# Kernel optimization log

Hardware: AMD Instinct MI355X
Metric: run time of the kernel (lower is better)

Reference implementation:

```python
import jax, jax.numpy as jnp
import numpy as np

NUM_NODES = 324
IN_DIM, HID_DIM, OUT_DIM = 128, 256, 64
BN_EPS = 1e-5
HUB_COLS = [7, 9, 24, 45, 59, 62, 63, 66, 67, 69, 70, 73, 74, 76, 77, 80, 81, 84,
            95, 97, 99, 114, 116, 118, 143, 147, 150, 152, 156, 158, 159, 163, 167, 171]


def _adj_norm() -> jnp.ndarray:
    """D^{-1/2} A D^{-1/2} for the fixed 324-node template graph (edge weights = 1)."""
    adj = np.eye(NUM_NODES, dtype=np.float32)
    cols = np.array(HUB_COLS)
    for r in range(300, NUM_NODES):
        adj[r, cols] = 1.0
        adj[cols, r] = 1.0
    deg = adj.sum(axis=1)
    dinv = 1.0 / np.sqrt(deg)
    return jnp.asarray(adj * dinv[:, None] * dinv[None, :])


def setup_inputs() -> dict:
    key = jax.random.key(0)
    ks = jax.random.split(key, 6)
    batch = 1024
    x = jax.random.normal(ks[0], (batch, NUM_NODES, IN_DIM), dtype=jnp.float32)
    # Xavier-uniform linear weights (PyG GCNConv lin has weight [out, in]), zero bias
    lim1 = float(np.sqrt(6.0 / (IN_DIM + HID_DIM)))
    W1 = jax.random.uniform(ks[1], (HID_DIM, IN_DIM), jnp.float32, -lim1, lim1)
    b1 = jnp.zeros((HID_DIM,), jnp.float32)
    lim2 = float(np.sqrt(6.0 / (HID_DIM + OUT_DIM)))
    W2 = jax.random.uniform(ks[2], (OUT_DIM, HID_DIM), jnp.float32, -lim2, lim2)
    b2 = jnp.zeros((OUT_DIM,), jnp.float32)
    # BatchNorm1d(hidden_dim) params + running stats (inference mode)
    gamma = jax.random.uniform(ks[3], (HID_DIM,), jnp.float32, 0.5, 1.5)
    beta = 0.1 * jax.random.normal(ks[4], (HID_DIM,), jnp.float32)
    running_mean = jnp.zeros((HID_DIM,), jnp.float32)
    running_var = jnp.ones((HID_DIM,), jnp.float32)
    return {"x": x, "W1": W1, "b1": b1, "W2": W2, "b2": b2,
            "gamma": gamma, "beta": beta,
            "running_mean": running_mean, "running_var": running_var,
            "adj_norm": _adj_norm()}


def reference(x, W1, b1, W2, b2, gamma, beta, running_mean, running_var, adj_norm):
    # Layer 0: GCNConv = aggregate(norm_adj, x @ W^T) + b  (batched over b)
    h = jnp.einsum("bnf,hf->bnh", x, W1)               # lin
    h = jnp.einsum("nm,bmh->bnh", adj_norm, h) + b1    # normalized scatter-aggregate
    h = jnp.where(h >= 0, h, 0.01 * h)                 # leaky_relu(0.01)
    # dropout: identity at inference
    h = (h - running_mean) * gamma * jax.lax.rsqrt(running_var + BN_EPS) + beta
    # Layer 1 (final): GCNConv only
    out = jnp.einsum("bnh,oh->bno", h, W2)
    out = jnp.einsum("nm,bmo->bno", adj_norm, out) + b2
    return out
```

## Files before the change

### kernel.cpp

```cpp
#include <hip/hip_runtime.h>

#define NN   324
#define INF  128
#define HID  256
#define OUTF 64

#define DINV_R 0.16903085f
#define DINV_H 0.2f

#define W1B_OFF 655360
#define W2B_OFF 671744
#define C2_OFF  679936

typedef float  f32x16 __attribute__((ext_vector_type(16)));
typedef short  short8 __attribute__((ext_vector_type(8)));

__constant__ int HUBC[34] = {7, 9, 24, 45, 59, 62, 63, 66, 67, 69, 70, 73, 74, 76,
                             77, 80, 81, 84, 95, 97, 99, 114, 116, 118, 143, 147,
                             150, 152, 156, 158, 159, 163, 167, 171};

#define HW0 ((1ULL<<7)|(1ULL<<9)|(1ULL<<24)|(1ULL<<45)|(1ULL<<59)|(1ULL<<62)|(1ULL<<63))
#define HW1 ((1ULL<<2)|(1ULL<<3)|(1ULL<<5)|(1ULL<<6)|(1ULL<<9)|(1ULL<<10)|(1ULL<<12)|(1ULL<<13)| \
             (1ULL<<16)|(1ULL<<17)|(1ULL<<20)|(1ULL<<31)|(1ULL<<33)|(1ULL<<35)|(1ULL<<50)|(1ULL<<52)|(1ULL<<54))
#define HW2 ((1ULL<<15)|(1ULL<<19)|(1ULL<<22)|(1ULL<<24)|(1ULL<<28)|(1ULL<<30)|(1ULL<<31)| \
             (1ULL<<35)|(1ULL<<39)|(1ULL<<43))

__device__ __forceinline__ bool is_hub(int n) {
    if (n >= 192) return false;
    unsigned long long w = (n < 64) ? HW0 : (n < 128 ? HW1 : HW2);
    return (w >> (n & 63)) & 1ULL;
}
__device__ __forceinline__ unsigned int f2bf1(float f) {
    unsigned int u = __builtin_bit_cast(unsigned int, f);
    return (u + 0x7fffu + ((u >> 16) & 1u)) >> 16;
}
__device__ __forceinline__ float bf2f(unsigned short h) {
    return __builtin_bit_cast(float, (unsigned int)h << 16);
}
__device__ __forceinline__ unsigned int f2bf2(float lo, float hi) {
    return f2bf1(lo) | (f2bf1(hi) << 16);
}
__device__ __forceinline__ uint4 pack8(float4 a, float4 b) {
    uint4 r;
    r.x = f2bf2(a.x, a.y); r.y = f2bf2(a.z, a.w);
    r.z = f2bf2(b.x, b.y); r.w = f2bf2(b.z, b.w);
    return r;
}
__device__ __forceinline__ short8 as_s8(uint4 u) {
    union { uint4 u; short8 s; } t; t.u = u; return t.s;
}

__global__ __launch_bounds__(256) void gcn_k00(
    const float* __restrict__ W1, const float* __restrict__ W2,
    const float* __restrict__ gamma, const float* __restrict__ beta,
    const float* __restrict__ rmean, const float* __restrict__ rvar,
    float* __restrict__ ws)
{
    const int blk = blockIdx.x, tid = threadIdx.x;
    if (blk < 16) {
        int p = blk * 256 + tid;
        int l31 = p & 31, hi = (p >> 5) & 1, ks = (p >> 6) & 7, htc = p >> 9;
        int h = htc * 32 + l31;
        int k0 = ks * 16 + hi * 8;
        const float4* s = (const float4*)(W1 + (size_t)h * INF + k0);
        ((uint4*)(ws + W1B_OFF))[p] = pack8(s[0], s[1]);
    } else if (blk < 24) {
        int p = (blk - 16) * 256 + tid;
        int l31 = p & 31, hi = (p >> 5) & 1, ot = (p >> 6) & 1, hs = (p >> 7) & 1, htc = p >> 8;
        int o = ot * 32 + l31;
        int h0 = htc * 32 + hs * 16 + hi * 8;
        float4 a = *(const float4*)(W2 + (size_t)o * HID + h0);
        float4 b = *(const float4*)(W2 + (size_t)o * HID + h0 + 4);
        float4 ga = *(const float4*)(gamma + h0), gb = *(const float4*)(gamma + h0 + 4);
        float4 va = *(const float4*)(rvar + h0),  vb = *(const float4*)(rvar + h0 + 4);
        a.x *= ga.x * rsqrtf(va.x + 1e-5f);  a.y *= ga.y * rsqrtf(va.y + 1e-5f);
        a.z *= ga.z * rsqrtf(va.z + 1e-5f);  a.w *= ga.w * rsqrtf(va.w + 1e-5f);
        b.x *= gb.x * rsqrtf(vb.x + 1e-5f);  b.y *= gb.y * rsqrtf(vb.y + 1e-5f);
        b.z *= gb.z * rsqrtf(vb.z + 1e-5f);  b.w *= gb.w * rsqrtf(vb.w + 1e-5f);
        ((uint4*)(ws + W2B_OFF))[p] = pack8(a, b);
    } else {
        if (tid < 64) {
            float s = 0.f;
            for (int h = 0; h < HID; ++h) {
                float sc  = gamma[h] * rsqrtf(rvar[h] + 1e-5f);
                float off = beta[h] - rmean[h] * sc;
                s += off * W2[(size_t)tid * HID + h];
            }
            ws[C2_OFF + tid] = s;
        }
    }
}

__global__ __launch_bounds__(256, 3) void gcn_k0(
    const float* __restrict__ x,  const float* __restrict__ b1,
    const float* __restrict__ W2, const float* __restrict__ gamma,
    const float* __restrict__ beta, const float* __restrict__ rmean,
    const float* __restrict__ rvar, float* __restrict__ ws)
{
    __shared__ uint4 Xs[16 * 67];
    __shared__ float sv1[2][256];
    __shared__ float vpart[2][2][256];
    __shared__ float vHl[2][256];

    const int tid = threadIdx.x, lane = tid & 63, w = tid >> 6;
    const int mt = w >> 1, nh = w & 1, l31 = lane & 31, hi = lane >> 5;
    const int b = blockIdx.x;
    const float* xb = x + (size_t)b * NN * INF;
    float* wsb = ws + (size_t)b * 640;
    const uint4* W1B2q = (const uint4*)(ws + W1B_OFF);

    for (int p = tid; p < 64 * 16; p += 256) {
        int lr = p >> 4, kg = p & 15;
        uint4 v = {0u, 0u, 0u, 0u};
        if (lr < 58) {
            int gr = (lr < 24) ? 300 + lr : HUBC[lr - 24];
            const float4* s = (const float4*)(xb + (size_t)gr * INF + kg * 8);
            v = pack8(s[0], s[1]);
        }
        Xs[kg * 67 + lr] = v;
    }
    __syncthreads();

    if (tid < 128) {
        int kg = tid >> 3, sub = tid & 7;
        const unsigned short* xs = (const unsigned short*)Xs;
        float s1 = 0.f, s2 = 0.f;
        for (int lr = 0; lr < 24; ++lr)  s1 += bf2f(xs[(kg * 67 + lr) * 8 + sub]);
        for (int lr = 24; lr < 58; ++lr) s2 += bf2f(xs[(kg * 67 + lr) * 8 + sub]);
        unsigned short* xw = (unsigned short*)Xs;
        xw[(kg * 67 + 58) * 8 + sub] = (unsigned short)f2bf1(s1 * DINV_R);
        xw[(kg * 67 + 59) * 8 + sub] = (unsigned short)f2bf1(s2 * DINV_H);
    }
    __syncthreads();

    f32x16 acc[4];
#pragma unroll
    for (int i = 0; i < 4; ++i)
#pragma unroll
        for (int j = 0; j < 16; ++j) acc[i][j] = 0.f;

#pragma unroll
    for (int ks = 0; ks < 8; ++ks) {
        short8 af = as_s8(Xs[(2 * ks + hi) * 67 + mt * 32 + l31]);
#pragma unroll
        for (int ntl = 0; ntl < 4; ++ntl) {
            short8 bf = as_s8(W1B2q[((nh * 4 + ntl) * 8 + ks) * 64 + lane]);
            acc[ntl] = __builtin_amdgcn_mfma_f32_32x32x16_bf16(af, bf, acc[ntl], 0, 0, 0);
        }
    }

    if (mt == 1 && hi == 0) {
#pragma unroll
        for (int ntl = 0; ntl < 4; ++ntl) {
            int col = nh * 128 + ntl * 32 + l31;
            float r58 = acc[ntl][14], r59 = acc[ntl][15];
            sv1[0][col] = r58;  sv1[1][col] = r59;
            wsb[col] = r58;     wsb[256 + col] = r59;
        }
    }
    __syncthreads();

    float p1[4] = {0.f, 0.f, 0.f, 0.f}, p2[4] = {0.f, 0.f, 0.f, 0.f};
#pragma unroll
    for (int ntl = 0; ntl < 4; ++ntl) {
        int col = nh * 128 + ntl * 32 + l31;
        float bias  = b1[col];
        float scale = gamma[col] * rsqrtf(rvar[col] + 1e-5f);
        float off   = beta[col] - rmean[col] * scale;
        float svA = sv1[0][col], svB = sv1[1][col];
#pragma unroll
        for (int q = 0; q < 16; ++q) {
            int lr = mt * 32 + (q & 3) + 8 * (q >> 2) + 4 * hi;
            bool isR = lr < 24, isH = (lr >= 24 && lr < 58);
            float d   = isR ? DINV_R : (isH ? DINV_H : 0.f);
            float oth = isR ? svB : svA;
            float v = d * d * acc[ntl][q] + d * oth + bias;
            v = fmaxf(v, 0.01f * v);
            float z = v * scale + off;
            p1[ntl] += isR ? DINV_R * z : 0.f;
            p2[ntl] += isH ? DINV_H * z : 0.f;
        }
    }
#pragma unroll
    for (int ntl = 0; ntl < 4; ++ntl) {
        p1[ntl] += __shfl_xor(p1[ntl], 32);
        p2[ntl] += __shfl_xor(p2[ntl], 32);
    }
    if (hi == 0) {
#pragma unroll
        for (int ntl = 0; ntl < 4; ++ntl) {
            int col = nh * 128 + ntl * 32 + l31;
            vpart[mt][0][col] = p1[ntl];
            vpart[mt][1][col] = p2[ntl];
        }
    }
    __syncthreads();
    for (int i = tid; i < 512; i += 256) {
        int which = i >> 8, col = i & 255;
        vHl[which][col] = vpart[0][which][col] + vpart[1][which][col];
    }
    __syncthreads();

    if (tid < 128) {
        int vr = tid >> 6, oc = tid & 63;
        const float* w2r = W2 + (size_t)oc * HID;
        float s = 0.f;
        for (int k = 0; k < 256; k += 8) {
#pragma unroll
            for (int i = 0; i < 8; ++i) s += vHl[vr][k + i] * w2r[k + i];
        }
        wsb[512 + vr * 64 + oc] = s;
    }
}

#define PSTR 33
#define LDS_XW  0
#define LDS_B1  33792
#define LDS_ST  34816
#define LDS_E2  36864
#define LDS_K1  37888
__global__ __launch_bounds__(256, 4) void gcn_k1(
    const float* __restrict__ x,  const float* __restrict__ b1,
    const float* __restrict__ b2, const float* __restrict__ ws,
    float* __restrict__ out)
{
    extern __shared__ char smem[];
    const int tid = threadIdx.x, lane = tid & 63, w = tid >> 6;
    const int l31 = lane & 31, hi = lane >> 5;
    uint4*  Xw  = (uint4*)(smem + LDS_XW) + w * (16 * PSTR);
    float*  eb1 = (float*)(smem + LDS_B1);
    float2* est = (float2*)(smem + LDS_ST);
    float4* e2t = (float4*)(smem + LDS_E2);

    const int bid = blockIdx.x;
    const int b = bid / 3, m3 = bid - b * 3;
    const int row0 = m3 * 128 + w * 32;
    const float* xb  = x + ((size_t)b * NN + row0) * INF;
    const float* wsb = ws + (size_t)b * 640;
    const uint4* W1q = (const uint4*)(ws + W1B_OFF);
    const uint4* W2q = (const uint4*)(ws + W2B_OFF);

    eb1[tid] = b1[tid];
    est[tid] = make_float2(wsb[tid], wsb[256 + tid]);
    if (tid < 64)
        e2t[tid] = make_float4(ws[C2_OFF + tid], wsb[512 + tid], wsb[576 + tid], b2[tid]);

    float tx, ty, tz;
    {
        int gr = row0 + l31;
        if (gr >= NN)        { tx = 0.f;               ty = 0.f;    tz = 0.f;    }
        else if (gr >= 300)  { tx = DINV_R * DINV_R;   ty = 0.f;    tz = DINV_R; }
        else if (is_hub(gr)) { tx = DINV_H * DINV_H;   ty = DINV_H; tz = 0.f;    }
        else                 { tx = 1.f;               ty = 0.f;    tz = 0.f;    }
    }
    const bool anyspec = __ballot((ty != 0.f) || (tz != 0.f)) != 0ULL;

#pragma unroll
    for (int i = 0; i < 8; ++i) {
        int p = lane + i * 64;
        int n = p >> 4, kg = p & 15;
        uint4 v = {0u, 0u, 0u, 0u};
        if (row0 + n < NN) {
            const float4* s = (const float4*)(xb + (size_t)n * INF + kg * 8);
            v = pack8(s[0], s[1]);
        }
        Xw[kg * PSTR + n] = v;
    }
    __syncthreads();

    f32x16 acc2a, acc2b;
#pragma unroll
    for (int j = 0; j < 16; ++j) { acc2a[j] = 0.f; acc2b[j] = 0.f; }

#pragma unroll
    for (int hc = 0; hc < 4; ++hc) {
#pragma unroll
        for (int j = 0; j < 2; ++j) {
            const int htc = hc * 2 + j;
            f32x16 acc1;
#pragma unroll
            for (int q = 0; q < 16; ++q) acc1[q] = 0.f;
            const uint4* w1 = W1q + (size_t)(htc * 8) * 64 + lane;
#pragma unroll
            for (int ks = 0; ks < 8; ++ks) {
                short8 bX = as_s8(Xw[(2 * ks + hi) * PSTR + l31]);
                acc1 = __builtin_amdgcn_mfma_f32_32x32x16_bf16(
                           as_s8(w1[ks * 64]), bX, acc1, 0, 0, 0);
            }
            float z[16];
            if (anyspec) {
#pragma unroll
                for (int q = 0; q < 16; ++q) {
                    int h = htc * 32 + (q & 3) + 8 * (q >> 2) + 4 * hi;
                    float2 st = est[h];
                    float v = tx * acc1[q] + ty * st.x + tz * st.y + eb1[h];
                    z[q] = fmaxf(v, 0.01f * v);
                }
            } else {
#pragma unroll
                for (int q = 0; q < 16; ++q) {
                    int h = htc * 32 + (q & 3) + 8 * (q >> 2) + 4 * hi;
                    float v = acc1[q] + eb1[h];
                    z[q] = fmaxf(v, 0.01f * v);
                }
            }
#pragma unroll
            for (int hs = 0; hs < 2; ++hs) {
                unsigned int a0 = f2bf2(z[8 * hs + 0], z[8 * hs + 1]);
                unsigned int a1 = f2bf2(z[8 * hs + 2], z[8 * hs + 3]);
                unsigned int a2 = f2bf2(z[8 * hs + 4], z[8 * hs + 5]);
                unsigned int a3 = f2bf2(z[8 * hs + 6], z[8 * hs + 7]);
                unsigned int s0 = __shfl_xor(a0, 32), s1 = __shfl_xor(a1, 32);
                unsigned int s2 = __shfl_xor(a2, 32), s3 = __shfl_xor(a3, 32);
                uint4 pz;
                pz.x = hi ? s2 : a0;
                pz.y = hi ? s3 : a1;
                pz.z = hi ? a2 : s0;
                pz.w = hi ? a3 : s1;
                short8 zb = as_s8(pz);
                short8 wa = as_s8(W2q[(size_t)(((htc * 2 + hs) * 2 + 0)) * 64 + lane]);
                short8 wb = as_s8(W2q[(size_t)(((htc * 2 + hs) * 2 + 1)) * 64 + lane]);
                acc2a = __builtin_amdgcn_mfma_f32_32x32x16_bf16(wa, zb, acc2a, 0, 0, 0);
                acc2b = __builtin_amdgcn_mfma_f32_32x32x16_bf16(wb, zb, acc2b, 0, 0, 0);
            }
        }
    }

    {
        float* Ol = (float*)Xw;
        if (anyspec) {
#pragma unroll
            for (int q = 0; q < 16; ++q) {
                int o = (q & 3) + 8 * (q >> 2) + 4 * hi;
                float4 ea = e2t[o], eb = e2t[32 + o];
                Ol[l31 * 65 + o]      = tx * (acc2a[q] + ea.x) + ty * ea.y + tz * ea.z + ea.w;
                Ol[l31 * 65 + 32 + o] = tx * (acc2b[q] + eb.x) + ty * eb.y + tz * eb.z + eb.w;
            }
        } else {
#pragma unroll
            for (int q = 0; q < 16; ++q) {
                int o = (q & 3) + 8 * (q >> 2) + 4 * hi;
                float4 ea = e2t[o], eb = e2t[32 + o];
                Ol[l31 * 65 + o]      = acc2a[q] + ea.x + ea.w;
                Ol[l31 * 65 + 32 + o] = acc2b[q] + eb.x + eb.w;
            }
        }
        const float* Olr = (const float*)Xw;
        float* ob = out + ((size_t)b * NN + row0) * OUTF;
#pragma unroll
        for (int i = 0; i < 8; ++i) {
            int p = lane + i * 64;
            int n = p >> 4, c4 = p & 15;
            if (row0 + n < NN) {
                float4 vv;
                vv.x = Olr[n * 65 + c4 * 4 + 0];
                vv.y = Olr[n * 65 + c4 * 4 + 1];
                vv.z = Olr[n * 65 + c4 * 4 + 2];
                vv.w = Olr[n * 65 + c4 * 4 + 3];
                *(float4*)(ob + (size_t)n * OUTF + c4 * 4) = vv;
            }
        }
    }
}

extern "C" void kernel_launch(void* const* d_in, const int* in_sizes, int n_in,
                              void* d_out, int out_size, void* d_ws, size_t ws_size,
                              hipStream_t stream) {
    const float* x     = (const float*)d_in[0];
    const float* W1    = (const float*)d_in[1];
    const float* b1    = (const float*)d_in[2];
    const float* W2    = (const float*)d_in[3];
    const float* b2    = (const float*)d_in[4];
    const float* gamma = (const float*)d_in[5];
    const float* beta  = (const float*)d_in[6];
    const float* rmean = (const float*)d_in[7];
    const float* rvar  = (const float*)d_in[8];
    float* out = (float*)d_out;
    float* ws  = (float*)d_ws;

    gcn_k00<<<dim3(25), dim3(256), 0, stream>>>(W1, W2, gamma, beta,
                                                rmean, rvar, ws);
    gcn_k0<<<dim3(1024), dim3(256), 0, stream>>>(x, b1, W2, gamma, beta,
                                                 rmean, rvar, ws);
    (void)hipFuncSetAttribute((const void*)gcn_k1,
                              hipFuncAttributeMaxDynamicSharedMemorySize, LDS_K1);
    gcn_k1<<<dim3(3072), dim3(256), LDS_K1, stream>>>(x, b1, b2, ws, out);
}
```

Baseline: 139.4 us.

## Load x fragments directly into registers and shrink LDS output staging

Each lane now loads and converts its own x fragment straight into registers in MFMA operand layout, instead of staging the tile through LDS and reading it back. The output transpose is split into two 32-column halves with a smaller per-wave LDS buffer, and LDS becomes static rather than dynamic. bf16 pair packing switches to the HIP intrinsic. This removes an LDS write/read round trip and cuts LDS footprint, which may raise occupancy. In exchange it costs 32 more VGPRs per lane, and the global loads become less coalesced because each lane reads 32-byte chunks strided by row.

Result: no change. 138.9 us, median of 2 (-0.4%).

```diff
diff --git a/kernel.cpp b/kernel.cpp
--- a/kernel.cpp
+++ b/kernel.cpp
@@ -1,4 +1,5 @@
 #include <hip/hip_runtime.h>
+#include <hip/hip_bf16.h>
 
 #define NN   324
 #define INF  128
@@ -38,7 +39,10 @@
     return __builtin_bit_cast(float, (unsigned int)h << 16);
 }
 __device__ __forceinline__ unsigned int f2bf2(float lo, float hi) {
-    return f2bf1(lo) | (f2bf1(hi) << 16);
+    __hip_bfloat162 h2 = __float22bfloat162_rn(make_float2(lo, hi));
+    unsigned int u;
+    __builtin_memcpy(&u, &h2, 4);
+    return u;
 }
 __device__ __forceinline__ uint4 pack8(float4 a, float4 b) {
     uint4 r;
@@ -213,24 +217,20 @@
     }
 }
 
-#define PSTR 33
-#define LDS_XW  0
-#define LDS_B1  33792
-#define LDS_ST  34816
-#define LDS_E2  36864
-#define LDS_K1  37888
+#define OSTR 33
 __global__ __launch_bounds__(256, 4) void gcn_k1(
     const float* __restrict__ x,  const float* __restrict__ b1,
     const float* __restrict__ b2, const float* __restrict__ ws,
     float* __restrict__ out)
 {
-    extern __shared__ char smem[];
+    __shared__ float  OlAll[4][32 * OSTR];
+    __shared__ float  eb1[256];
+    __shared__ float2 est[256];
+    __shared__ float4 e2t[64];
+
     const int tid = threadIdx.x, lane = tid & 63, w = tid >> 6;
     const int l31 = lane & 31, hi = lane >> 5;
-    uint4*  Xw  = (uint4*)(smem + LDS_XW) + w * (16 * PSTR);
-    float*  eb1 = (float*)(smem + LDS_B1);
-    float2* est = (float2*)(smem + LDS_ST);
-    float4* e2t = (float4*)(smem + LDS_E2);
+    float* Ol = OlAll[w];
 
     const int bid = blockIdx.x;
     const int b = bid / 3, m3 = bid - b * 3;
@@ -255,16 +255,16 @@
     }
     const bool anyspec = __ballot((ty != 0.f) || (tz != 0.f)) != 0ULL;
 
-#pragma unroll
-    for (int i = 0; i < 8; ++i) {
-        int p = lane + i * 64;
-        int n = p >> 4, kg = p & 15;
+    const bool rowok = (row0 + l31 < NN);
+    uint4 xf[8];
+#pragma unroll
+    for (int ks = 0; ks < 8; ++ks) {
         uint4 v = {0u, 0u, 0u, 0u};
-        if (row0 + n < NN) {
-            const float4* s = (const float4*)(xb + (size_t)n * INF + kg * 8);
+        if (rowok) {
+            const float4* s = (const float4*)(xb + (size_t)l31 * INF + (2 * ks + hi) * 8);
             v = pack8(s[0], s[1]);
         }
-        Xw[kg * PSTR + n] = v;
+        xf[ks] = v;
     }
     __syncthreads();
 
@@ -283,9 +283,8 @@
             const uint4* w1 = W1q + (size_t)(htc * 8) * 64 + lane;
 #pragma unroll
             for (int ks = 0; ks < 8; ++ks) {
-                short8 bX = as_s8(Xw[(2 * ks + hi) * PSTR + l31]);
                 acc1 = __builtin_amdgcn_mfma_f32_32x32x16_bf16(
-                           as_s8(w1[ks * 64]), bX, acc1, 0, 0, 0);
+                           as_s8(w1[ks * 64]), as_s8(xf[ks]), acc1, 0, 0, 0);
             }
             float z[16];
             if (anyspec) {
@@ -326,38 +325,36 @@
         }
     }
 
-    {
-        float* Ol = (float*)Xw;
+    float* ob = out + ((size_t)b * NN + row0) * OUTF;
+#pragma unroll
+    for (int half = 0; half < 2; ++half) {
+        const f32x16& acc = half ? acc2b : acc2a;
         if (anyspec) {
 #pragma unroll
             for (int q = 0; q < 16; ++q) {
                 int o = (q & 3) + 8 * (q >> 2) + 4 * hi;
-                float4 ea = e2t[o], eb = e2t[32 + o];
-                Ol[l31 * 65 + o]      = tx * (acc2a[q] + ea.x) + ty * ea.y + tz * ea.z + ea.w;
-                Ol[l31 * 65 + 32 + o] = tx * (acc2b[q] + eb.x) + ty * eb.y + tz * eb.z + eb.w;
+                float4 e = e2t[half * 32 + o];
+                Ol[l31 * OSTR + o] = tx * (acc[q] + e.x) + ty * e.y + tz * e.z + e.w;
             }
         } else {
 #pragma unroll
             for (int q = 0; q < 16; ++q) {
                 int o = (q & 3) + 8 * (q >> 2) + 4 * hi;
-                float4 ea = e2t[o], eb = e2t[32 + o];
-                Ol[l31 * 65 + o]      = acc2a[q] + ea.x + ea.w;
-                Ol[l31 * 65 + 32 + o] = acc2b[q] + eb.x + eb.w;
-            }
-        }
-        const float* Olr = (const float*)Xw;
-        float* ob = out + ((size_t)b * NN + row0) * OUTF;
-#pragma unroll
-        for (int i = 0; i < 8; ++i) {
+                float4 e = e2t[half * 32 + o];
+                Ol[l31 * OSTR + o] = acc[q] + e.x + e.w;
+            }
+        }
+#pragma unroll
+        for (int i = 0; i < 4; ++i) {
             int p = lane + i * 64;
-            int n = p >> 4, c4 = p & 15;
+            int n = p >> 3, c4 = p & 7;
             if (row0 + n < NN) {
                 float4 vv;
-                vv.x = Olr[n * 65 + c4 * 4 + 0];
-                vv.y = Olr[n * 65 + c4 * 4 + 1];
-                vv.z = Olr[n * 65 + c4 * 4 + 2];
-                vv.w = Olr[n * 65 + c4 * 4 + 3];
-                *(float4*)(ob + (size_t)n * OUTF + c4 * 4) = vv;
+                vv.x = Ol[n * OSTR + c4 * 4 + 0];
+                vv.y = Ol[n * OSTR + c4 * 4 + 1];
+                vv.z = Ol[n * OSTR + c4 * 4 + 2];
+                vv.w = Ol[n * OSTR + c4 * 4 + 3];
+                *(float4*)(ob + (size_t)n * OUTF + half * 32 + c4 * 4) = vv;
             }
         }
     }
@@ -382,7 +379,5 @@
                                                 rmean, rvar, ws);
     gcn_k0<<<dim3(1024), dim3(256), 0, stream>>>(x, b1, W2, gamma, beta,
                                                  rmean, rvar, ws);
-    (void)hipFuncSetAttribute((const void*)gcn_k1,
-                              hipFuncAttributeMaxDynamicSharedMemorySize, LDS_K1);
-    gcn_k1<<<dim3(3072), dim3(256), LDS_K1, stream>>>(x, b1, b2, ws, out);
-}
+    gcn_k1<<<dim3(3072), dim3(256), 0, stream>>>(x, b1, b2, ws, out);
+}
```
